# Kernel optimization log

Hardware: AMD Instinct MI355X
Metric: run time of the kernel (lower is better)

Reference implementation:

```python
import jax, jax.numpy as jnp
import numpy as np

NC = 10        # output capsule classes
R = 2048       # num_routes (input capsules)
IN_DIM = 8
OUT_DIM = 16
ITERS = 3
EPS = 1e-8


def squash(s):
    # norm / (1 + norm^2 + eps) * s, over last dim
    norm = jnp.linalg.norm(s, axis=-1, keepdims=True)
    return norm / (1.0 + norm ** 2 + EPS) * s


def setup_inputs() -> dict:
    key = jax.random.key(0)
    k1, k2 = jax.random.split(key)
    x = jax.random.normal(k1, (256, R, IN_DIM), dtype=jnp.float32)
    # W ~ N(0,1) per reset_params
    W = jax.random.normal(k2, (R, IN_DIM, NC * OUT_DIM), dtype=jnp.float32)
    # routing logits b initialized to zeros
    b = jnp.zeros((R, NC), dtype=jnp.float32)
    return {"x": x, "W": W, "b": b}


def reference(x, W, b):
    B = x.shape[0]
    # u_hat: [B, R, NC, OUT_DIM] = x[b,r,:] @ W[r,:,:]
    u_hat = jnp.einsum('bri,rio->bro', x, W).reshape(B, R, NC, OUT_DIM)
    # initial coupling from learned logits b (softmax over classes)
    c = jax.nn.softmax(b, axis=-1)                      # [R, NC]
    s = jnp.sum(c[None, :, :, None] * u_hat, axis=1)    # [B, NC, OUT_DIM]
    v = squash(s)
    # dynamic routing
    bB = jnp.broadcast_to(b, (B, R, NC))
    for _ in range(ITERS):
        # agreement: dot(u_hat, v) over OUT_DIM
        bB = bB + jnp.sum(u_hat * v[:, None, :, :], axis=-1)   # [B, R, NC]
        c = jax.nn.softmax(bB, axis=-1)                          # [B, R, NC]
        s = jnp.sum(c[..., None] * u_hat, axis=1)                # [B, NC, OUT_DIM]
        v = squash(s)
    return v, c
```

## Files before the change

### kernel.cpp

```cpp
#include <hip/hip_runtime.h>
#include <hip/hip_fp16.h>
#include <cstdint>
#include <cstddef>


#define B_   256
#define R_   2048
#define NC_  10
#define OD_  16
#define IN_  8

__device__ __forceinline__ float rsum16(float x){
  x += __shfl_xor(x, 1, 16);
  x += __shfl_xor(x, 2, 16);
  x += __shfl_xor(x, 4, 16);
  x += __shfl_xor(x, 8, 16);
  return x;
}
__device__ __forceinline__ float rmax16(float x){
  x = fmaxf(x, __shfl_xor(x, 1, 16));
  x = fmaxf(x, __shfl_xor(x, 2, 16));
  x = fmaxf(x, __shfl_xor(x, 4, 16));
  x = fmaxf(x, __shfl_xor(x, 8, 16));
  return x;
}
__device__ __forceinline__ unsigned pack_f16(float a, float b){
  __half2 h = __floats2half2_rn(a, b);
  return *(unsigned*)&h;
}
__device__ __forceinline__ void unpack8(uint4 d, float* f){
  float2 t;
  t = __half22float2(*(__half2*)&d.x); f[0] = t.x; f[1] = t.y;
  t = __half22float2(*(__half2*)&d.y); f[2] = t.x; f[3] = t.y;
  t = __half22float2(*(__half2*)&d.z); f[4] = t.x; f[5] = t.y;
  t = __half22float2(*(__half2*)&d.w); f[6] = t.x; f[7] = t.y;
}

__global__ __launch_bounds__(256) void c0_kernel(const float* __restrict__ b_in,
                                                 float* __restrict__ c0){
  int r = blockIdx.x * 256 + threadIdx.x;
  if (r >= R_) return;
  float t[NC_];
  float m = -1e30f;
  #pragma unroll
  for (int n = 0; n < NC_; ++n){ t[n] = b_in[r * NC_ + n]; m = fmaxf(m, t[n]); }
  float sum = 0.f;
  #pragma unroll
  for (int n = 0; n < NC_; ++n){ t[n] = __expf(t[n] - m); sum += t[n]; }
  float inv = 1.f / sum;
  #pragma unroll
  for (int n = 0; n < NC_; ++n) c0[r * NC_ + n] = t[n] * inv;
}

__global__ __launch_bounds__(256) void uhat_kernel(const float* __restrict__ x,
                                                   const float* __restrict__ W,
                                                   uint32_t* __restrict__ U){
  const int r = blockIdx.x;
  __shared__ float Wl[IN_ * 160];
  {
    const float4* Wg = (const float4*)(W + (size_t)r * (IN_ * 160));
    float4* Wl4 = (float4*)Wl;
    for (int i = threadIdx.x; i < (IN_ * 160) / 4; i += 256) Wl4[i] = Wg[i];
  }
  __syncthreads();
  const int b = threadIdx.x;
  const float4* xp = (const float4*)(x + ((size_t)b * R_ + r) * IN_);
  float4 xa = xp[0], xb = xp[1];
  float xr[8] = {xa.x, xa.y, xa.z, xa.w, xb.x, xb.y, xb.z, xb.w};
  uint32_t* out = U + (((size_t)b * R_ + r) * 160) / 2;
  const float4* Wl4 = (const float4*)Wl;
  #pragma unroll 4
  for (int co = 0; co < 40; ++co){
    float4 u = make_float4(0.f, 0.f, 0.f, 0.f);
    #pragma unroll
    for (int i = 0; i < 8; ++i){
      float4 w = Wl4[i * 40 + co];
      u.x = fmaf(xr[i], w.x, u.x);
      u.y = fmaf(xr[i], w.y, u.y);
      u.z = fmaf(xr[i], w.z, u.z);
      u.w = fmaf(xr[i], w.w, u.w);
    }
    uint2 p; p.x = pack_f16(u.x, u.y); p.y = pack_f16(u.z, u.w);
    ((uint2*)out)[co] = p;
  }
}

template<int MODE>
__global__ __launch_bounds__(256) void pass_kernel(
    const uint32_t* __restrict__ U,
    const float*    __restrict__ c0,
    const float*    __restrict__ b_in,
    float*          __restrict__ bB,
    const float*    __restrict__ v,
    float*          __restrict__ s)
{
  const int b  = blockIdx.x >> 3;
  const int rc = blockIdx.x & 7;
  const int n  = threadIdx.x & 15;
  const int rs = threadIdx.x >> 4;
  const int nn = (n < NC_) ? n : (NC_ - 1);

  float vreg[16];
  if (MODE != 0){
    const float* vp = v + b * 160 + nn * 16;
    #pragma unroll
    for (int o = 0; o < 16; ++o) vreg[o] = vp[o];
  }
  float acc[16];
  #pragma unroll
  for (int o = 0; o < 16; ++o) acc[o] = 0.f;

  const int r0 = rc * 256;
  for (int rr = 0; rr < 16; ++rr){
    const int r = r0 + rr * 16 + rs;
    const size_t row = (size_t)b * R_ + r;
    const uint4* up = (const uint4*)(U + row * 80 + n * 8);
    float uf[16];
    unpack8(up[0], uf);
    unpack8(up[1], uf + 8);

    float c;
    if (MODE == 0){
      c = c0[r * NC_ + nn];
      if (n >= NC_) c = 0.f;
    } else {
      float t = 0.f;
      #pragma unroll
      for (int o = 0; o < 16; ++o) t = fmaf(uf[o], vreg[o], t);
      float bold = (MODE == 1) ? b_in[r * NC_ + nn] : bB[row * NC_ + nn];
      float bnew = (n < NC_) ? (bold + t) : -1e30f;
      float m = rmax16(bnew);
      float e = __expf(bnew - m);
      float sum = rsum16(e);
      c = e / sum;
      if (MODE == 3){
        if (n < NC_) bB[row * NC_ + n] = c;
      } else {
        if (n < NC_) bB[row * NC_ + n] = bnew;
      }
    }
    #pragma unroll
    for (int o = 0; o < 16; ++o) acc[o] = fmaf(c, uf[o], acc[o]);
  }

  __shared__ float sd[16 * 16 * 17];
  #pragma unroll
  for (int o = 0; o < 16; ++o) sd[rs * 272 + n * 17 + o] = acc[o];
  __syncthreads();
  const int n2 = threadIdx.x >> 4;
  const int o2 = threadIdx.x & 15;
  if (n2 < NC_){
    float tot = 0.f;
    #pragma unroll
    for (int k = 0; k < 16; ++k) tot += sd[k * 272 + n2 * 17 + o2];
    atomicAdd(&s[b * 160 + n2 * 16 + o2], tot);
  }
}

template<bool FINAL>
__global__ __launch_bounds__(256) void squash_kernel(float* __restrict__ s,
                                                     float* __restrict__ vout){
  int g = blockIdx.x * 256 + threadIdx.x;
  float xv = s[g];
  float ss = rsum16(xv * xv);
  float norm = sqrtf(ss);
  float f = norm / (1.f + ss + 1e-8f);
  vout[g] = f * xv;
  if (!FINAL) s[g] = 0.f;
}

extern "C" void kernel_launch(void* const* d_in, const int* in_sizes, int n_in,
                              void* d_out, int out_size, void* d_ws, size_t ws_size,
                              hipStream_t stream){
  const float* x    = (const float*)d_in[0];
  const float* W    = (const float*)d_in[1];
  const float* b_in = (const float*)d_in[2];
  float* out = (float*)d_out;
  float* out_v = out;
  float* bB    = out + 40960;

  char* w = (char*)d_ws;
  uint32_t* U = (uint32_t*)w;
  float* s  = (float*)(w + 167772160);
  float* v  = (float*)(w + 167772160 + 163840);
  float* c0 = (float*)(w + 167772160 + 2 * 163840);

  hipMemsetAsync(s, 0, 40960 * sizeof(float), stream);
  c0_kernel<<<8, 256, 0, stream>>>(b_in, c0);
  uhat_kernel<<<R_, 256, 0, stream>>>(x, W, U);

  pass_kernel<0><<<2048, 256, 0, stream>>>(U, c0, b_in, bB, v, s);
  squash_kernel<false><<<160, 256, 0, stream>>>(s, v);
  pass_kernel<1><<<2048, 256, 0, stream>>>(U, c0, b_in, bB, v, s);
  squash_kernel<false><<<160, 256, 0, stream>>>(s, v);
  pass_kernel<2><<<2048, 256, 0, stream>>>(U, c0, b_in, bB, v, s);
  squash_kernel<false><<<160, 256, 0, stream>>>(s, v);
  pass_kernel<3><<<2048, 256, 0, stream>>>(U, c0, b_in, bB, v, s);
  squash_kernel<true><<<160, 256, 0, stream>>>(s, out_v);
}
```

Before: 270.8 us.

## Recompute u_hat on the fly in each routing pass instead of materializing fp16 U

Removes the separate u_hat kernel and its large fp16 intermediate buffer. Each routing pass now recomputes u_hat from x and W, with blocks tiled over 16 batches by 16 routes. The atomic accumulation into s is replaced by per-route-tile partial sums, which a combined reduce+squash kernel sums deterministically. This trades heavy U reads (about 168MB per pass) for redundant FMA work and more W/x reads, and adds a 21MB partial buffer per pass.

```diff
diff --git a/kernel.cpp b/kernel.cpp
--- a/kernel.cpp
+++ b/kernel.cpp
@@ -1,5 +1,4 @@
 #include <hip/hip_runtime.h>
-#include <hip/hip_fp16.h>
 #include <cstdint>
 #include <cstddef>
 
@@ -7,8 +6,8 @@
 #define B_   256
 #define R_   2048
 #define NC_  10
-#define OD_  16
-#define IN_  8
+#define TR_  16
+#define NRT_ 128
 
 __device__ __forceinline__ float rsum16(float x){
   x += __shfl_xor(x, 1, 16);
@@ -23,17 +22,6 @@
   x = fmaxf(x, __shfl_xor(x, 4, 16));
   x = fmaxf(x, __shfl_xor(x, 8, 16));
   return x;
-}
-__device__ __forceinline__ unsigned pack_f16(float a, float b){
-  __half2 h = __floats2half2_rn(a, b);
-  return *(unsigned*)&h;
-}
-__device__ __forceinline__ void unpack8(uint4 d, float* f){
-  float2 t;
-  t = __half22float2(*(__half2*)&d.x); f[0] = t.x; f[1] = t.y;
-  t = __half22float2(*(__half2*)&d.y); f[2] = t.x; f[3] = t.y;
-  t = __half22float2(*(__half2*)&d.z); f[4] = t.x; f[5] = t.y;
-  t = __half22float2(*(__half2*)&d.w); f[6] = t.x; f[7] = t.y;
 }
 
 __global__ __launch_bounds__(256) void c0_kernel(const float* __restrict__ b_in,
@@ -52,121 +40,111 @@
   for (int n = 0; n < NC_; ++n) c0[r * NC_ + n] = t[n] * inv;
 }
 
-__global__ __launch_bounds__(256) void uhat_kernel(const float* __restrict__ x,
-                                                   const float* __restrict__ W,
-                                                   uint32_t* __restrict__ U){
-  const int r = blockIdx.x;
-  __shared__ float Wl[IN_ * 160];
-  {
-    const float4* Wg = (const float4*)(W + (size_t)r * (IN_ * 160));
-    float4* Wl4 = (float4*)Wl;
-    for (int i = threadIdx.x; i < (IN_ * 160) / 4; i += 256) Wl4[i] = Wg[i];
-  }
-  __syncthreads();
-  const int b = threadIdx.x;
-  const float4* xp = (const float4*)(x + ((size_t)b * R_ + r) * IN_);
-  float4 xa = xp[0], xb = xp[1];
-  float xr[8] = {xa.x, xa.y, xa.z, xa.w, xb.x, xb.y, xb.z, xb.w};
-  uint32_t* out = U + (((size_t)b * R_ + r) * 160) / 2;
-  const float4* Wl4 = (const float4*)Wl;
-  #pragma unroll 4
-  for (int co = 0; co < 40; ++co){
-    float4 u = make_float4(0.f, 0.f, 0.f, 0.f);
-    #pragma unroll
-    for (int i = 0; i < 8; ++i){
-      float4 w = Wl4[i * 40 + co];
-      u.x = fmaf(xr[i], w.x, u.x);
-      u.y = fmaf(xr[i], w.y, u.y);
-      u.z = fmaf(xr[i], w.z, u.z);
-      u.w = fmaf(xr[i], w.w, u.w);
-    }
-    uint2 p; p.x = pack_f16(u.x, u.y); p.y = pack_f16(u.z, u.w);
-    ((uint2*)out)[co] = p;
-  }
-}
-
 template<int MODE>
 __global__ __launch_bounds__(256) void pass_kernel(
-    const uint32_t* __restrict__ U,
-    const float*    __restrict__ c0,
-    const float*    __restrict__ b_in,
-    float*          __restrict__ bB,
-    const float*    __restrict__ v,
-    float*          __restrict__ s)
+    const float* __restrict__ x,
+    const float* __restrict__ W,
+    const float* __restrict__ c0,
+    const float* __restrict__ b_in,
+    float*       __restrict__ bB,
+    const float* __restrict__ v,
+    float*       __restrict__ P)
 {
-  const int b  = blockIdx.x >> 3;
-  const int rc = blockIdx.x & 7;
+  const int bt = blockIdx.x >> 7;
+  const int rt = blockIdx.x & 127;
   const int n  = threadIdx.x & 15;
-  const int rs = threadIdx.x >> 4;
+  const int bs = threadIdx.x >> 4;
+  const int b  = bt * 16 + bs;
   const int nn = (n < NC_) ? n : (NC_ - 1);
 
   float vreg[16];
   if (MODE != 0){
-    const float* vp = v + b * 160 + nn * 16;
-    #pragma unroll
-    for (int o = 0; o < 16; ++o) vreg[o] = vp[o];
+    const float4* vp = (const float4*)(v + b * 160 + nn * 16);
+    float4 v0 = vp[0], v1 = vp[1], v2 = vp[2], v3 = vp[3];
+    vreg[0]=v0.x; vreg[1]=v0.y; vreg[2]=v0.z; vreg[3]=v0.w;
+    vreg[4]=v1.x; vreg[5]=v1.y; vreg[6]=v1.z; vreg[7]=v1.w;
+    vreg[8]=v2.x; vreg[9]=v2.y; vreg[10]=v2.z; vreg[11]=v2.w;
+    vreg[12]=v3.x; vreg[13]=v3.y; vreg[14]=v3.z; vreg[15]=v3.w;
   }
   float acc[16];
   #pragma unroll
   for (int o = 0; o < 16; ++o) acc[o] = 0.f;
 
-  const int r0 = rc * 256;
-  for (int rr = 0; rr < 16; ++rr){
-    const int r = r0 + rr * 16 + rs;
-    const size_t row = (size_t)b * R_ + r;
-    const uint4* up = (const uint4*)(U + row * 80 + n * 8);
-    float uf[16];
-    unpack8(up[0], uf);
-    unpack8(up[1], uf + 8);
+  const int r0 = rt * TR_;
+  #pragma unroll 2
+  for (int j = 0; j < TR_; ++j){
+    const int r = r0 + j;
+    const float4* xp = (const float4*)(x + ((size_t)b * R_ + r) * 8);
+    float4 xa = xp[0], xb = xp[1];
+    float xr[8] = {xa.x, xa.y, xa.z, xa.w, xb.x, xb.y, xb.z, xb.w};
+    float u[16];
+    #pragma unroll
+    for (int o = 0; o < 16; ++o) u[o] = 0.f;
+    const float4* Wp = (const float4*)(W + (size_t)r * 1280 + nn * 16);
+    #pragma unroll
+    for (int i = 0; i < 8; ++i){
+      float4 w0 = Wp[i * 40 + 0];
+      float4 w1 = Wp[i * 40 + 1];
+      float4 w2 = Wp[i * 40 + 2];
+      float4 w3 = Wp[i * 40 + 3];
+      const float xi = xr[i];
+      u[0]  = fmaf(xi, w0.x, u[0]);  u[1]  = fmaf(xi, w0.y, u[1]);
+      u[2]  = fmaf(xi, w0.z, u[2]);  u[3]  = fmaf(xi, w0.w, u[3]);
+      u[4]  = fmaf(xi, w1.x, u[4]);  u[5]  = fmaf(xi, w1.y, u[5]);
+      u[6]  = fmaf(xi, w1.z, u[6]);  u[7]  = fmaf(xi, w1.w, u[7]);
+      u[8]  = fmaf(xi, w2.x, u[8]);  u[9]  = fmaf(xi, w2.y, u[9]);
+      u[10] = fmaf(xi, w2.z, u[10]); u[11] = fmaf(xi, w2.w, u[11]);
+      u[12] = fmaf(xi, w3.x, u[12]); u[13] = fmaf(xi, w3.y, u[13]);
+      u[14] = fmaf(xi, w3.z, u[14]); u[15] = fmaf(xi, w3.w, u[15]);
+    }
 
     float c;
     if (MODE == 0){
-      c = c0[r * NC_ + nn];
-      if (n >= NC_) c = 0.f;
+      c = (n < NC_) ? c0[r * NC_ + nn] : 0.f;
     } else {
       float t = 0.f;
       #pragma unroll
-      for (int o = 0; o < 16; ++o) t = fmaf(uf[o], vreg[o], t);
+      for (int o = 0; o < 16; ++o) t = fmaf(u[o], vreg[o], t);
+      const size_t row = (size_t)b * R_ + r;
       float bold = (MODE == 1) ? b_in[r * NC_ + nn] : bB[row * NC_ + nn];
       float bnew = (n < NC_) ? (bold + t) : -1e30f;
       float m = rmax16(bnew);
       float e = __expf(bnew - m);
       float sum = rsum16(e);
       c = e / sum;
-      if (MODE == 3){
-        if (n < NC_) bB[row * NC_ + n] = c;
-      } else {
-        if (n < NC_) bB[row * NC_ + n] = bnew;
+      if (n < NC_){
+        if (MODE == 3) bB[row * NC_ + n] = c;
+        else           bB[row * NC_ + n] = bnew;
       }
     }
     #pragma unroll
-    for (int o = 0; o < 16; ++o) acc[o] = fmaf(c, uf[o], acc[o]);
+    for (int o = 0; o < 16; ++o) acc[o] = fmaf(c, u[o], acc[o]);
   }
 
-  __shared__ float sd[16 * 16 * 17];
-  #pragma unroll
-  for (int o = 0; o < 16; ++o) sd[rs * 272 + n * 17 + o] = acc[o];
-  __syncthreads();
-  const int n2 = threadIdx.x >> 4;
-  const int o2 = threadIdx.x & 15;
-  if (n2 < NC_){
-    float tot = 0.f;
-    #pragma unroll
-    for (int k = 0; k < 16; ++k) tot += sd[k * 272 + n2 * 17 + o2];
-    atomicAdd(&s[b * 160 + n2 * 16 + o2], tot);
+  if (n < NC_){
+    float4* Pp = (float4*)(P + ((size_t)rt * B_ + b) * 160 + n * 16);
+    Pp[0] = make_float4(acc[0],  acc[1],  acc[2],  acc[3]);
+    Pp[1] = make_float4(acc[4],  acc[5],  acc[6],  acc[7]);
+    Pp[2] = make_float4(acc[8],  acc[9],  acc[10], acc[11]);
+    Pp[3] = make_float4(acc[12], acc[13], acc[14], acc[15]);
   }
 }
 
-template<bool FINAL>
-__global__ __launch_bounds__(256) void squash_kernel(float* __restrict__ s,
+__global__ __launch_bounds__(256) void reduce_squash(const float* __restrict__ P,
                                                      float* __restrict__ vout){
   int g = blockIdx.x * 256 + threadIdx.x;
-  float xv = s[g];
-  float ss = rsum16(xv * xv);
-  float norm = sqrtf(ss);
-  float f = norm / (1.f + ss + 1e-8f);
-  vout[g] = f * xv;
-  if (!FINAL) s[g] = 0.f;
+  float s0 = 0.f, s1 = 0.f, s2 = 0.f, s3 = 0.f;
+  #pragma unroll 4
+  for (int j = 0; j < NRT_; j += 4){
+    s0 += P[(size_t)(j + 0) * 40960 + g];
+    s1 += P[(size_t)(j + 1) * 40960 + g];
+    s2 += P[(size_t)(j + 2) * 40960 + g];
+    s3 += P[(size_t)(j + 3) * 40960 + g];
+  }
+  float sv = (s0 + s1) + (s2 + s3);
+  float ss = rsum16(sv * sv);
+  float f = sqrtf(ss) / (1.f + ss + 1e-8f);
+  vout[g] = f * sv;
 }
 
 extern "C" void kernel_launch(void* const* d_in, const int* in_sizes, int n_in,
@@ -175,26 +153,23 @@
   const float* x    = (const float*)d_in[0];
   const float* W    = (const float*)d_in[1];
   const float* b_in = (const float*)d_in[2];
-  float* out = (float*)d_out;
+  float* out   = (float*)d_out;
   float* out_v = out;
   float* bB    = out + 40960;
 
   char* w = (char*)d_ws;
-  uint32_t* U = (uint32_t*)w;
-  float* s  = (float*)(w + 167772160);
-  float* v  = (float*)(w + 167772160 + 163840);
-  float* c0 = (float*)(w + 167772160 + 2 * 163840);
+  float* P  = (float*)w;
+  float* v  = (float*)(w + (size_t)NRT_ * B_ * 160 * 4);
+  float* c0 = (float*)(w + (size_t)NRT_ * B_ * 160 * 4 + 163840);
 
-  hipMemsetAsync(s, 0, 40960 * sizeof(float), stream);
   c0_kernel<<<8, 256, 0, stream>>>(b_in, c0);
-  uhat_kernel<<<R_, 256, 0, stream>>>(x, W, U);
 
-  pass_kernel<0><<<2048, 256, 0, stream>>>(U, c0, b_in, bB, v, s);
-  squash_kernel<false><<<160, 256, 0, stream>>>(s, v);
-  pass_kernel<1><<<2048, 256, 0, stream>>>(U, c0, b_in, bB, v, s);
-  squash_kernel<false><<<160, 256, 0, stream>>>(s, v);
-  pass_kernel<2><<<2048, 256, 0, stream>>>(U, c0, b_in, bB, v, s);
-  squash_kernel<false><<<160, 256, 0, stream>>>(s, v);
-  pass_kernel<3><<<2048, 256, 0, stream>>>(U, c0, b_in, bB, v, s);
-  squash_kernel<true><<<160, 256, 0, stream>>>(s, out_v);
+  pass_kernel<0><<<2048, 256, 0, stream>>>(x, W, c0, b_in, bB, v, P);
+  reduce_squash<<<160, 256, 0, stream>>>(P, v);
+  pass_kernel<1><<<2048, 256, 0, stream>>>(x, W, c0, b_in, bB, v, P);
+  reduce_squash<<<160, 256, 0, stream>>>(P, v);
+  pass_kernel<2><<<2048, 256, 0, stream>>>(x, W, c0, b_in, bB, v, P);
+  reduce_squash<<<160, 256, 0, stream>>>(P, v);
+  pass_kernel<3><<<2048, 256, 0, stream>>>(x, W, c0, b_in, bB, v, P);
+  reduce_squash<<<160, 256, 0, stream>>>(P, out_v);
 }
```

Result: slower. 887.7 us (+227.8%).

## Store u_hat route-major and give each pass block 16 batches over 32 routes

Applied to the files above, without the earlier changes.

The u_hat buffer layout changes from [b][r] to [r][b], so a warp's loads across consecutive batches hit contiguous memory, and the u_hat kernel writes 16-byte packets. The pass kernel now assigns 16 batches times 32 routes per block with 1024 blocks, so each thread accumulates its own batch's s. The shared-memory reduction is dropped in favour of per-thread atomicAdds, which multiplies global atomic traffic. Reads and writes of bB stay batch-major, so those accesses become strided.

```diff
diff --git a/kernel.cpp b/kernel.cpp
--- a/kernel.cpp
+++ b/kernel.cpp
@@ -7,8 +7,6 @@
 #define B_   256
 #define R_   2048
 #define NC_  10
-#define OD_  16
-#define IN_  8
 
 __device__ __forceinline__ float rsum16(float x){
   x += __shfl_xor(x, 1, 16);
@@ -56,32 +54,36 @@
                                                    const float* __restrict__ W,
                                                    uint32_t* __restrict__ U){
   const int r = blockIdx.x;
-  __shared__ float Wl[IN_ * 160];
+  __shared__ float Wl[8 * 160];
   {
-    const float4* Wg = (const float4*)(W + (size_t)r * (IN_ * 160));
+    const float4* Wg = (const float4*)(W + (size_t)r * 1280);
     float4* Wl4 = (float4*)Wl;
-    for (int i = threadIdx.x; i < (IN_ * 160) / 4; i += 256) Wl4[i] = Wg[i];
+    for (int i = threadIdx.x; i < 320; i += 256) Wl4[i] = Wg[i];
   }
   __syncthreads();
   const int b = threadIdx.x;
-  const float4* xp = (const float4*)(x + ((size_t)b * R_ + r) * IN_);
+  const float4* xp = (const float4*)(x + ((size_t)b * R_ + r) * 8);
   float4 xa = xp[0], xb = xp[1];
   float xr[8] = {xa.x, xa.y, xa.z, xa.w, xb.x, xb.y, xb.z, xb.w};
-  uint32_t* out = U + (((size_t)b * R_ + r) * 160) / 2;
+  uint4* out4 = (uint4*)(U + ((size_t)r * B_ + b) * 80);
   const float4* Wl4 = (const float4*)Wl;
   #pragma unroll 4
-  for (int co = 0; co < 40; ++co){
-    float4 u = make_float4(0.f, 0.f, 0.f, 0.f);
+  for (int c8 = 0; c8 < 20; ++c8){
+    float u[8] = {0.f,0.f,0.f,0.f,0.f,0.f,0.f,0.f};
     #pragma unroll
     for (int i = 0; i < 8; ++i){
-      float4 w = Wl4[i * 40 + co];
-      u.x = fmaf(xr[i], w.x, u.x);
-      u.y = fmaf(xr[i], w.y, u.y);
-      u.z = fmaf(xr[i], w.z, u.z);
-      u.w = fmaf(xr[i], w.w, u.w);
+      float4 w0 = Wl4[i * 40 + c8 * 2];
+      float4 w1 = Wl4[i * 40 + c8 * 2 + 1];
+      const float xi = xr[i];
+      u[0] = fmaf(xi, w0.x, u[0]); u[1] = fmaf(xi, w0.y, u[1]);
+      u[2] = fmaf(xi, w0.z, u[2]); u[3] = fmaf(xi, w0.w, u[3]);
+      u[4] = fmaf(xi, w1.x, u[4]); u[5] = fmaf(xi, w1.y, u[5]);
+      u[6] = fmaf(xi, w1.z, u[6]); u[7] = fmaf(xi, w1.w, u[7]);
     }
-    uint2 p; p.x = pack_f16(u.x, u.y); p.y = pack_f16(u.z, u.w);
-    ((uint2*)out)[co] = p;
+    uint4 pkt;
+    pkt.x = pack_f16(u[0], u[1]); pkt.y = pack_f16(u[2], u[3]);
+    pkt.z = pack_f16(u[4], u[5]); pkt.w = pack_f16(u[6], u[7]);
+    out4[c8] = pkt;
   }
 }
 
@@ -94,66 +96,61 @@
     const float*    __restrict__ v,
     float*          __restrict__ s)
 {
-  const int b  = blockIdx.x >> 3;
-  const int rc = blockIdx.x & 7;
+  const int bt = blockIdx.x >> 6;
+  const int rc = blockIdx.x & 63;
   const int n  = threadIdx.x & 15;
-  const int rs = threadIdx.x >> 4;
+  const int bs = threadIdx.x >> 4;
+  const int b  = bt * 16 + bs;
   const int nn = (n < NC_) ? n : (NC_ - 1);
 
   float vreg[16];
   if (MODE != 0){
-    const float* vp = v + b * 160 + nn * 16;
-    #pragma unroll
-    for (int o = 0; o < 16; ++o) vreg[o] = vp[o];
+    const float4* vp = (const float4*)(v + b * 160 + nn * 16);
+    float4 v0 = vp[0], v1 = vp[1], v2 = vp[2], v3 = vp[3];
+    vreg[0]=v0.x; vreg[1]=v0.y; vreg[2]=v0.z; vreg[3]=v0.w;
+    vreg[4]=v1.x; vreg[5]=v1.y; vreg[6]=v1.z; vreg[7]=v1.w;
+    vreg[8]=v2.x; vreg[9]=v2.y; vreg[10]=v2.z; vreg[11]=v2.w;
+    vreg[12]=v3.x; vreg[13]=v3.y; vreg[14]=v3.z; vreg[15]=v3.w;
   }
   float acc[16];
   #pragma unroll
   for (int o = 0; o < 16; ++o) acc[o] = 0.f;
 
-  const int r0 = rc * 256;
-  for (int rr = 0; rr < 16; ++rr){
-    const int r = r0 + rr * 16 + rs;
-    const size_t row = (size_t)b * R_ + r;
-    const uint4* up = (const uint4*)(U + row * 80 + n * 8);
+  const int r0 = rc * 32;
+  for (int j = 0; j < 32; ++j){
+    const int r = r0 + j;
+    const uint4* up = (const uint4*)(U + ((size_t)r * B_ + b) * 80 + nn * 8);
     float uf[16];
     unpack8(up[0], uf);
     unpack8(up[1], uf + 8);
 
     float c;
     if (MODE == 0){
-      c = c0[r * NC_ + nn];
-      if (n >= NC_) c = 0.f;
+      c = (n < NC_) ? c0[r * NC_ + nn] : 0.f;
     } else {
       float t = 0.f;
       #pragma unroll
       for (int o = 0; o < 16; ++o) t = fmaf(uf[o], vreg[o], t);
+      const size_t row = (size_t)b * R_ + r;
       float bold = (MODE == 1) ? b_in[r * NC_ + nn] : bB[row * NC_ + nn];
       float bnew = (n < NC_) ? (bold + t) : -1e30f;
       float m = rmax16(bnew);
       float e = __expf(bnew - m);
       float sum = rsum16(e);
       c = e / sum;
-      if (MODE == 3){
-        if (n < NC_) bB[row * NC_ + n] = c;
-      } else {
-        if (n < NC_) bB[row * NC_ + n] = bnew;
+      if (n < NC_){
+        if (MODE == 3) bB[row * NC_ + n] = c;
+        else           bB[row * NC_ + n] = bnew;
       }
     }
     #pragma unroll
     for (int o = 0; o < 16; ++o) acc[o] = fmaf(c, uf[o], acc[o]);
   }
 
-  __shared__ float sd[16 * 16 * 17];
-  #pragma unroll
-  for (int o = 0; o < 16; ++o) sd[rs * 272 + n * 17 + o] = acc[o];
-  __syncthreads();
-  const int n2 = threadIdx.x >> 4;
-  const int o2 = threadIdx.x & 15;
-  if (n2 < NC_){
-    float tot = 0.f;
+  if (n < NC_){
+    float* sp = s + b * 160 + n * 16;
     #pragma unroll
-    for (int k = 0; k < 16; ++k) tot += sd[k * 272 + n2 * 17 + o2];
-    atomicAdd(&s[b * 160 + n2 * 16 + o2], tot);
+    for (int o = 0; o < 16; ++o) atomicAdd(sp + o, acc[o]);
   }
 }
 
@@ -163,8 +160,7 @@
   int g = blockIdx.x * 256 + threadIdx.x;
   float xv = s[g];
   float ss = rsum16(xv * xv);
-  float norm = sqrtf(ss);
-  float f = norm / (1.f + ss + 1e-8f);
+  float f = sqrtf(ss) / (1.f + ss + 1e-8f);
   vout[g] = f * xv;
   if (!FINAL) s[g] = 0.f;
 }
@@ -175,7 +171,7 @@
   const float* x    = (const float*)d_in[0];
   const float* W    = (const float*)d_in[1];
   const float* b_in = (const float*)d_in[2];
-  float* out = (float*)d_out;
+  float* out   = (float*)d_out;
   float* out_v = out;
   float* bB    = out + 40960;
 
@@ -189,12 +185,12 @@
   c0_kernel<<<8, 256, 0, stream>>>(b_in, c0);
   uhat_kernel<<<R_, 256, 0, stream>>>(x, W, U);
 
-  pass_kernel<0><<<2048, 256, 0, stream>>>(U, c0, b_in, bB, v, s);
+  pass_kernel<0><<<1024, 256, 0, stream>>>(U, c0, b_in, bB, v, s);
   squash_kernel<false><<<160, 256, 0, stream>>>(s, v);
-  pass_kernel<1><<<2048, 256, 0, stream>>>(U, c0, b_in, bB, v, s);
+  pass_kernel<1><<<1024, 256, 0, stream>>>(U, c0, b_in, bB, v, s);
   squash_kernel<false><<<160, 256, 0, stream>>>(s, v);
-  pass_kernel<2><<<2048, 256, 0, stream>>>(U, c0, b_in, bB, v, s);
+  pass_kernel<2><<<1024, 256, 0, stream>>>(U, c0, b_in, bB, v, s);
   squash_kernel<false><<<160, 256, 0, stream>>>(s, v);
-  pass_kernel<3><<<2048, 256, 0, stream>>>(U, c0, b_in, bB, v, s);
+  pass_kernel<3><<<1024, 256, 0, stream>>>(U, c0, b_in, bB, v, s);
   squash_kernel<true><<<160, 256, 0, stream>>>(s, out_v);
 }
```

New measurement: 971.6 us. 3.59x slower.
